# Kernel optimization log

Measured on AMD Instinct MI355X. Metric: run time of the kernel, lower is better.

The kernel has to match this reference:

```python
import jax, jax.numpy as jnp
import numpy as np

KEY_BITS = 1024
VALUE_BITS = 1024
CAPACITY = 65536
BATCH = 2048


def setup_inputs() -> dict:
    key = jax.random.key(0)
    kq, kk, kv = jax.random.split(key, 3)
    query = jax.random.randint(kq, (BATCH, KEY_BITS), 0, 2, dtype=jnp.int32)
    keys = jax.random.randint(kk, (CAPACITY, KEY_BITS), 0, 2, dtype=jnp.int32)
    values = jax.random.normal(kv, (CAPACITY, VALUE_BITS), dtype=jnp.float32)
    return {"query": query, "keys": keys, "values": values}


def reference(query, keys, values):
    # Hamming mismatches between 0/1 bit vectors via GEMM:
    #   popcount(q ^ k) = sum(q) + sum(k) - 2 * (q . k)
    qf = query.astype(jnp.float32)                      # [B, key_bits]
    kf = keys.astype(jnp.float32)                       # [C, key_bits]
    dot = jnp.einsum('bk,ck->bc', qf, kf)               # [B, C]
    mismatches = qf.sum(axis=1, keepdims=True) + kf.sum(axis=1)[None, :] - 2.0 * dot
    sim = KEY_BITS - mismatches                         # similarity = key_bits - Hamming dist
    best_idx = jnp.argmax(sim, axis=1)                  # first max, matches strict '>' loop
    return values[best_idx]                             # [B, value_bits]
```

## Files before the change

kernel.cpp:

```cpp
#include <hip/hip_runtime.h>
#include <stdint.h>

typedef int v4i  __attribute__((ext_vector_type(4)));
typedef int v16i __attribute__((ext_vector_type(16)));

#define CAPACITY  65536
#define BATCH     2048
#define KBITS     1024
#define NSTEP     16
#define NBUF      3


__global__ void prep_qT_kernel(const int* __restrict__ in,
                               uint32_t* __restrict__ outT) {
    const int row = blockIdx.x, t = threadIdx.x;
    int4 v = reinterpret_cast<const int4*>(in)[(size_t)row * 256 + t];
    uint32_t b = (uint32_t)(v.x & 1)        | ((uint32_t)(v.y & 1) << 8) |
                 ((uint32_t)(v.z & 1) << 16) | ((uint32_t)(v.w & 1) << 24);
    outT[(size_t)(t >> 2) * (BATCH * 4) + (size_t)row * 4 + (t & 3)] = b;
}

__global__ void prep_i8_kernel(const int* __restrict__ in,
                               unsigned char* __restrict__ out8,
                               int* __restrict__ sums) {
    const int row = blockIdx.x, t = threadIdx.x;
    int4 v = reinterpret_cast<const int4*>(in)[(size_t)row * 256 + t];
    uint32_t b = (uint32_t)(v.x & 1)        | ((uint32_t)(v.y & 1) << 8) |
                 ((uint32_t)(v.z & 1) << 16) | ((uint32_t)(v.w & 1) << 24);
    reinterpret_cast<uint32_t*>(out8)[(size_t)row * 256 + t] = b;
    int s = (v.x & 1) + (v.y & 1) + (v.z & 1) + (v.w & 1);
    for (int off = 32; off; off >>= 1) s += __shfl_xor(s, off, 64);
    __shared__ int ws4[4];
    if ((t & 63) == 0) ws4[t >> 6] = s;
    __syncthreads();
    if (t == 0) sums[row] = ws4[0] + ws4[1] + ws4[2] + ws4[3];
}

__global__ void init_best_kernel(uint32_t* __restrict__ best) {
    best[blockIdx.x * 256 + threadIdx.x] = 0xFFFFFFFFu;
}

__device__ __forceinline__ int swz(int idx) { return idx ^ ((idx >> 3) & 7); }

__launch_bounds__(256, 4)
__global__ void gemm_scan_kernel(const uint4* __restrict__ aT4,
                                 const unsigned char* __restrict__ ki8,
                                 const int* __restrict__ sumk,
                                 uint32_t* __restrict__ best) {
    __shared__ uint4 sB[NBUF][512];

    const int t    = threadIdx.x;
    const int lane = t & 63, wid = t >> 6;
    const int wr   = wid >> 1, wc = wid & 1;
    const int ln   = lane & 31, kh = lane >> 5;

    const int b     = blockIdx.x;
    const int slot  = b >> 3;
    const int ntile = (b & 7) * 64 + (slot >> 4);
    const int mtile = slot & 15;
    const int m0 = mtile * 128, n0 = ntile * 128;

    const unsigned char* bSrc[2];
#pragma unroll
    for (int i = 0; i < 2; ++i) {
        int idx = swz(i * 256 + t);
        bSrc[i] = ki8 + (size_t)(n0 + (idx >> 2)) * KBITS + (idx & 3) * 16;
    }
    auto STAGE_B = [&](int buf, int kc) {
#pragma unroll
        for (int i = 0; i < 2; ++i)
            __builtin_amdgcn_global_load_lds(
                (const __attribute__((address_space(1))) void*)(bSrc[i] + kc),
                (__attribute__((address_space(3))) void*)&sB[buf][i * 256 + wid * 64],
                16, 0, 0);
    };

    int offB[2][2];
#pragma unroll
    for (int km = 0; km < 2; ++km)
#pragma unroll
        for (int ct = 0; ct < 2; ++ct)
            offB[km][ct] = swz((wc * 64 + ct * 32 + ln) * 4 + km * 2 + kh);

    const int mbase = m0 + wr * 64 + ln;

    v16i acc[2][2];
#pragma unroll
    for (int rt = 0; rt < 2; ++rt)
#pragma unroll
        for (int ct = 0; ct < 2; ++ct)
#pragma unroll
            for (int e = 0; e < 16; ++e) acc[rt][ct][e] = 0;

    STAGE_B(0, 0);
    STAGE_B(1, 64);
    asm volatile("s_waitcnt vmcnt(2)" ::: "memory");
    __builtin_amdgcn_s_barrier();

    int buf = 0;
    for (int s = 0; s < NSTEP; ++s) {
        uint4 af[2][2];
#pragma unroll
        for (int km = 0; km < 2; ++km)
#pragma unroll
            for (int rt = 0; rt < 2; ++rt)
                af[km][rt] = aT4[(size_t)(s * 4 + km * 2 + kh) * BATCH
                                 + mbase + rt * 32];

        if (s + 2 < NSTEP) {
            int nb = buf + 2; if (nb >= NBUF) nb -= NBUF;
            STAGE_B(nb, (s + 2) * 64);
        }

        uint4 bf[2][2];
#pragma unroll
        for (int km = 0; km < 2; ++km)
#pragma unroll
            for (int ct = 0; ct < 2; ++ct) bf[km][ct] = sB[buf][offB[km][ct]];

        __builtin_amdgcn_s_setprio(1);
#pragma unroll
        for (int rt = 0; rt < 2; ++rt)
#pragma unroll
            for (int ct = 0; ct < 2; ++ct)
                acc[rt][ct] = __builtin_amdgcn_mfma_i32_32x32x32_i8(
                    *(v4i*)&af[0][rt], *(v4i*)&bf[0][ct], acc[rt][ct], 0, 0, 0);
        __builtin_amdgcn_s_setprio(0);
        __builtin_amdgcn_s_setprio(1);
#pragma unroll
        for (int rt = 0; rt < 2; ++rt)
#pragma unroll
            for (int ct = 0; ct < 2; ++ct)
                acc[rt][ct] = __builtin_amdgcn_mfma_i32_32x32x32_i8(
                    *(v4i*)&af[1][rt], *(v4i*)&bf[1][ct], acc[rt][ct], 0, 0, 0);
        __builtin_amdgcn_s_setprio(0);

        if (s < NSTEP - 1) {
            if (s < NSTEP - 2)
                asm volatile("s_waitcnt vmcnt(2) lgkmcnt(0)" ::: "memory");
            else
                asm volatile("s_waitcnt vmcnt(0) lgkmcnt(0)" ::: "memory");
            __builtin_amdgcn_s_barrier();
        }
        buf = buf + 1 == NBUF ? 0 : buf + 1;
    }

    int sk[2];
#pragma unroll
    for (int ct = 0; ct < 2; ++ct) sk[ct] = sumk[n0 + wc * 64 + ct * 32 + ln];

#pragma unroll
    for (int rt = 0; rt < 2; ++rt) {
#pragma unroll
        for (int r = 0; r < 16; ++r) {
            const int qrow = m0 + wr * 64 + rt * 32 + (r & 3) + 8 * (r >> 2) + 4 * kh;
            uint32_t bmin = 0xFFFFFFFFu;
#pragma unroll
            for (int ct = 0; ct < 2; ++ct) {
                uint32_t dist = (uint32_t)(sk[ct] - 2 * acc[rt][ct][r] + 2048);
                uint32_t col  = (uint32_t)(n0 + wc * 64 + ct * 32 + ln);
                bmin = min(bmin, (dist << 16) | col);
            }
#pragma unroll
            for (int off = 1; off < 32; off <<= 1)
                bmin = min(bmin, (uint32_t)__shfl_xor((int)bmin, off, 64));
            if (ln == 0) atomicMin(&best[qrow], bmin);
        }
    }
}

__global__ void finalize_kernel(const uint32_t* __restrict__ best,
                                const float* __restrict__ values,
                                float* __restrict__ out) {
    const int qy  = blockIdx.x;
    const int idx = (int)(best[qy] & 0xFFFFu);
    const float4* v4 = reinterpret_cast<const float4*>(values) + (size_t)idx * 256;
    float4* o4 = reinterpret_cast<float4*>(out) + (size_t)qy * 256;
    o4[threadIdx.x] = v4[threadIdx.x];
}

#define KCHUNK 256
#define NSPLIT (CAPACITY / KCHUNK)

__device__ __forceinline__ uint32_t pack_word(const int4* __restrict__ p) {
    uint32_t word = 0;
#pragma unroll
    for (int j = 0; j < 8; ++j) {
        int4 v = p[j];
        word |= (uint32_t)(v.x & 1) << (4 * j + 0);
        word |= (uint32_t)(v.y & 1) << (4 * j + 1);
        word |= (uint32_t)(v.z & 1) << (4 * j + 2);
        word |= (uint32_t)(v.w & 1) << (4 * j + 3);
    }
    return word;
}

__global__ void pack_bits_kernel(const int* __restrict__ in,
                                 uint32_t* __restrict__ out, int nwords) {
    int w = blockIdx.x * blockDim.x + threadIdx.x;
    if (w >= nwords) return;
    out[w] = pack_word(reinterpret_cast<const int4*>(in) + (size_t)w * 8);
}

__launch_bounds__(256, 4)
__global__ void scan_kernel(const uint32_t* __restrict__ qpack,
                            const uint32_t* __restrict__ kpack,
                            uint32_t* __restrict__ best) {
    const int t      = threadIdx.x;
    const int lane   = t & 63;
    const int wid    = t >> 6;
    const int ksplit = blockIdx.x & (NSPLIT - 1);
    const int qgb    = blockIdx.x >> 8;
    const int query  = qgb * 256 + wid * 64 + lane;

    uint32_t q[32];
    const uint4* qp4 = reinterpret_cast<const uint4*>(qpack + (size_t)query * 32);
#pragma unroll
    for (int j = 0; j < 8; ++j) {
        uint4 v = qp4[j];
        q[4 * j + 0] = v.x; q[4 * j + 1] = v.y;
        q[4 * j + 2] = v.z; q[4 * j + 3] = v.w;
    }
    uint32_t bst = 0xFFFFFFFFu;
    const int k0 = ksplit * KCHUNK;
#pragma unroll 2
    for (int k = k0; k < k0 + KCHUNK; ++k) {
        const uint4* kw4 = reinterpret_cast<const uint4*>(kpack + (size_t)k * 32);
        uint32_t dist = 0;
#pragma unroll
        for (int j = 0; j < 8; ++j) {
            uint4 kv = kw4[j];
            dist += __popc(kv.x ^ q[4 * j + 0]);
            dist += __popc(kv.y ^ q[4 * j + 1]);
            dist += __popc(kv.z ^ q[4 * j + 2]);
            dist += __popc(kv.w ^ q[4 * j + 3]);
        }
        bst = min(bst, (dist << 16) | (uint32_t)k);
    }
    atomicMin(&best[query], bst);
}

extern "C" void kernel_launch(void* const* d_in, const int* in_sizes, int n_in,
                              void* d_out, int out_size, void* d_ws, size_t ws_size,
                              hipStream_t stream) {
    const int*   query  = (const int*)d_in[0];
    const int*   keys   = (const int*)d_in[1];
    const float* values = (const float*)d_in[2];
    float*       out    = (float*)d_out;
    char* ws = (char*)d_ws;

    const size_t need = 2097152ULL + 67108864ULL + 262144ULL + 8192ULL;
    if (ws_size >= need) {
        uint32_t* qT  = (uint32_t*)ws;
        unsigned char* ki8 = (unsigned char*)(ws + 2097152);
        int* sumk = (int*)(ws + 2097152 + 67108864);
        uint32_t* best = (uint32_t*)(ws + 2097152 + 67108864 + 262144);

        init_best_kernel<<<BATCH / 256, 256, 0, stream>>>(best);
        prep_qT_kernel<<<BATCH,    256, 0, stream>>>(query, qT);
        prep_i8_kernel<<<CAPACITY, 256, 0, stream>>>(keys, ki8, sumk);
        gemm_scan_kernel<<<16 * 512, 256, 0, stream>>>(
            reinterpret_cast<const uint4*>(qT), ki8, sumk, best);
        finalize_kernel<<<BATCH, 256, 0, stream>>>(best, values, out);
    } else {
        uint32_t* qpack = (uint32_t*)ws;
        uint32_t* kpack = (uint32_t*)(ws + 262144);
        uint32_t* best  = (uint32_t*)(ws + 262144 + 8388608);

        init_best_kernel<<<BATCH / 256, 256, 0, stream>>>(best);
        pack_bits_kernel<<<BATCH * 32 / 256, 256, 0, stream>>>(query, qpack, BATCH * 32);
        pack_bits_kernel<<<CAPACITY * 32 / 256, 256, 0, stream>>>(keys, kpack, CAPACITY * 32);
        scan_kernel<<<8 * NSPLIT, 256, 0, stream>>>(qpack, kpack, best);
        finalize_kernel<<<BATCH, 256, 0, stream>>>(best, values, out);
    }
}
```

Baseline: 277.4 us.

## Shrink GEMM-scan blocks to single-wave 64x64 tiles with barrier-free double buffering

Replaces 256-thread blocks computing 128x128 tiles with 64-thread single-wave blocks computing 64x64 tiles. The grid grows four times, the LDS ring drops from three buffers to two, and the workgroup barriers go away because one wave owns its own staged B data. The goal is to remove barrier stalls and raise scheduling flexibility. In exchange, B tiles are reused across fewer rows, so global and L2 traffic for both operands doubles, and there are more atomicMin operations per query row.

```diff
diff --git a/kernel.cpp b/kernel.cpp
--- a/kernel.cpp
+++ b/kernel.cpp
@@ -8,7 +8,6 @@
 #define BATCH     2048
 #define KBITS     1024
 #define NSTEP     16
-#define NBUF      3
 
 
 __global__ void prep_qT_kernel(const int* __restrict__ in,
@@ -42,36 +41,34 @@
 
 __device__ __forceinline__ int swz(int idx) { return idx ^ ((idx >> 3) & 7); }
 
-__launch_bounds__(256, 4)
+__launch_bounds__(64, 4)
 __global__ void gemm_scan_kernel(const uint4* __restrict__ aT4,
                                  const unsigned char* __restrict__ ki8,
                                  const int* __restrict__ sumk,
                                  uint32_t* __restrict__ best) {
-    __shared__ uint4 sB[NBUF][512];
+    __shared__ uint4 sB[2][256];
 
     const int t    = threadIdx.x;
-    const int lane = t & 63, wid = t >> 6;
-    const int wr   = wid >> 1, wc = wid & 1;
-    const int ln   = lane & 31, kh = lane >> 5;
+    const int ln   = t & 31, kh = t >> 5;
 
     const int b     = blockIdx.x;
     const int slot  = b >> 3;
-    const int ntile = (b & 7) * 64 + (slot >> 4);
-    const int mtile = slot & 15;
-    const int m0 = mtile * 128, n0 = ntile * 128;
-
-    const unsigned char* bSrc[2];
-#pragma unroll
-    for (int i = 0; i < 2; ++i) {
-        int idx = swz(i * 256 + t);
+    const int mtile = slot >> 7;
+    const int ntile = (b & 7) * 128 + (slot & 127);
+    const int m0 = mtile * 64, n0 = ntile * 64;
+
+    const unsigned char* bSrc[4];
+#pragma unroll
+    for (int i = 0; i < 4; ++i) {
+        int idx = swz(i * 64 + t);
         bSrc[i] = ki8 + (size_t)(n0 + (idx >> 2)) * KBITS + (idx & 3) * 16;
     }
     auto STAGE_B = [&](int buf, int kc) {
 #pragma unroll
-        for (int i = 0; i < 2; ++i)
+        for (int i = 0; i < 4; ++i)
             __builtin_amdgcn_global_load_lds(
                 (const __attribute__((address_space(1))) void*)(bSrc[i] + kc),
-                (__attribute__((address_space(3))) void*)&sB[buf][i * 256 + wid * 64],
+                (__attribute__((address_space(3))) void*)&sB[buf][i * 64],
                 16, 0, 0);
     };
 
@@ -80,9 +77,9 @@
     for (int km = 0; km < 2; ++km)
 #pragma unroll
         for (int ct = 0; ct < 2; ++ct)
-            offB[km][ct] = swz((wc * 64 + ct * 32 + ln) * 4 + km * 2 + kh);
-
-    const int mbase = m0 + wr * 64 + ln;
+            offB[km][ct] = swz((ct * 32 + ln) * 4 + km * 2 + kh);
+
+    const int mbase = m0 + ln;
 
     v16i acc[2][2];
 #pragma unroll
@@ -94,11 +91,18 @@
 
     STAGE_B(0, 0);
     STAGE_B(1, 64);
-    asm volatile("s_waitcnt vmcnt(2)" ::: "memory");
-    __builtin_amdgcn_s_barrier();
-
-    int buf = 0;
+    asm volatile("s_waitcnt vmcnt(4)" ::: "memory");
+
+#pragma unroll
     for (int s = 0; s < NSTEP; ++s) {
+        const int buf = s & 1;
+
+        uint4 bf[2][2];
+#pragma unroll
+        for (int km = 0; km < 2; ++km)
+#pragma unroll
+            for (int ct = 0; ct < 2; ++ct) bf[km][ct] = sB[buf][offB[km][ct]];
+
         uint4 af[2][2];
 #pragma unroll
         for (int km = 0; km < 2; ++km)
@@ -107,58 +111,38 @@
                 af[km][rt] = aT4[(size_t)(s * 4 + km * 2 + kh) * BATCH
                                  + mbase + rt * 32];
 
-        if (s + 2 < NSTEP) {
-            int nb = buf + 2; if (nb >= NBUF) nb -= NBUF;
-            STAGE_B(nb, (s + 2) * 64);
-        }
-
-        uint4 bf[2][2];
+        asm volatile("s_waitcnt lgkmcnt(0)" ::: "memory");
+        if (s + 2 < NSTEP) STAGE_B(buf, (s + 2) * 64);
+
+        if (s + 2 < NSTEP)
+            asm volatile("s_waitcnt vmcnt(4)" ::: "memory");
+        else
+            asm volatile("s_waitcnt vmcnt(0)" ::: "memory");
+
 #pragma unroll
         for (int km = 0; km < 2; ++km)
 #pragma unroll
-            for (int ct = 0; ct < 2; ++ct) bf[km][ct] = sB[buf][offB[km][ct]];
-
-        __builtin_amdgcn_s_setprio(1);
-#pragma unroll
-        for (int rt = 0; rt < 2; ++rt)
-#pragma unroll
-            for (int ct = 0; ct < 2; ++ct)
-                acc[rt][ct] = __builtin_amdgcn_mfma_i32_32x32x32_i8(
-                    *(v4i*)&af[0][rt], *(v4i*)&bf[0][ct], acc[rt][ct], 0, 0, 0);
-        __builtin_amdgcn_s_setprio(0);
-        __builtin_amdgcn_s_setprio(1);
-#pragma unroll
-        for (int rt = 0; rt < 2; ++rt)
-#pragma unroll
-            for (int ct = 0; ct < 2; ++ct)
-                acc[rt][ct] = __builtin_amdgcn_mfma_i32_32x32x32_i8(
-                    *(v4i*)&af[1][rt], *(v4i*)&bf[1][ct], acc[rt][ct], 0, 0, 0);
-        __builtin_amdgcn_s_setprio(0);
-
-        if (s < NSTEP - 1) {
-            if (s < NSTEP - 2)
-                asm volatile("s_waitcnt vmcnt(2) lgkmcnt(0)" ::: "memory");
-            else
-                asm volatile("s_waitcnt vmcnt(0) lgkmcnt(0)" ::: "memory");
-            __builtin_amdgcn_s_barrier();
-        }
-        buf = buf + 1 == NBUF ? 0 : buf + 1;
+            for (int rt = 0; rt < 2; ++rt)
+#pragma unroll
+                for (int ct = 0; ct < 2; ++ct)
+                    acc[rt][ct] = __builtin_amdgcn_mfma_i32_32x32x32_i8(
+                        *(v4i*)&af[km][rt], *(v4i*)&bf[km][ct], acc[rt][ct], 0, 0, 0);
     }
 
     int sk[2];
 #pragma unroll
-    for (int ct = 0; ct < 2; ++ct) sk[ct] = sumk[n0 + wc * 64 + ct * 32 + ln];
+    for (int ct = 0; ct < 2; ++ct) sk[ct] = sumk[n0 + ct * 32 + ln];
 
 #pragma unroll
     for (int rt = 0; rt < 2; ++rt) {
 #pragma unroll
         for (int r = 0; r < 16; ++r) {
-            const int qrow = m0 + wr * 64 + rt * 32 + (r & 3) + 8 * (r >> 2) + 4 * kh;
+            const int qrow = m0 + rt * 32 + (r & 3) + 8 * (r >> 2) + 4 * kh;
             uint32_t bmin = 0xFFFFFFFFu;
 #pragma unroll
             for (int ct = 0; ct < 2; ++ct) {
                 uint32_t dist = (uint32_t)(sk[ct] - 2 * acc[rt][ct][r] + 2048);
-                uint32_t col  = (uint32_t)(n0 + wc * 64 + ct * 32 + ln);
+                uint32_t col  = (uint32_t)(n0 + ct * 32 + ln);
                 bmin = min(bmin, (dist << 16) | col);
             }
 #pragma unroll
@@ -259,7 +243,7 @@
         init_best_kernel<<<BATCH / 256, 256, 0, stream>>>(best);
         prep_qT_kernel<<<BATCH,    256, 0, stream>>>(query, qT);
         prep_i8_kernel<<<CAPACITY, 256, 0, stream>>>(keys, ki8, sumk);
-        gemm_scan_kernel<<<16 * 512, 256, 0, stream>>>(
+        gemm_scan_kernel<<<32 * 1024, 64, 0, stream>>>(
             reinterpret_cast<const uint4*>(qT), ki8, sumk, best);
         finalize_kernel<<<BATCH, 256, 0, stream>>>(best, values, out);
     } else {
```

After: 885.0 us. +219.0%, slower.
